# Kernel optimization log

Measured on AMD Instinct MI355X. Metric: run time of the kernel, lower is better.

## Reference

```python
import jax, jax.numpy as jnp
import numpy as np
from jax import lax

BN_EPS = 1e-5
DELTA_FRAC = 0.7


def ternarize(t):
    """Per-row (dim 0) ternarization: delta = 0.7*mean|t_i|, alpha = mean of |t_i| above delta."""
    B = t.shape[0]
    flat = t.reshape(B, -1)                       # [B, n]
    absf = jnp.abs(flat)
    n = flat.shape[1]
    d = DELTA_FRAC * absf.sum(axis=1) / n         # [B]
    mask = absf > d[:, None]                      # strict >, matching torch code
    count = mask.sum(axis=1).astype(flat.dtype)
    alpha = (absf * mask).sum(axis=1) / count     # [B]
    tern = jnp.where(flat > d[:, None], 1.0, 0.0) + jnp.where(flat < -d[:, None], -1.0, 0.0)
    return (tern * alpha[:, None]).reshape(t.shape)


def conv2d(x, w, b):
    out = lax.conv_general_dilated(x, w, window_strides=(1, 1), padding='VALID',
                                   dimension_numbers=('NCHW', 'OIHW', 'NCHW'))
    return out + b[None, :, None, None]


def maxpool2(x):
    return lax.reduce_window(x, -jnp.inf, lax.max, (1, 1, 2, 2), (1, 1, 2, 2), 'VALID')


def batchnorm_eval(x, gamma, beta):
    # eval-mode BN with running_mean=0, running_var=1
    inv = 1.0 / np.sqrt(1.0 + BN_EPS)
    return x * (gamma[None, :, None, None] * inv) + beta[None, :, None, None]


def setup_inputs() -> dict:
    key = jax.random.key(0)
    ks = jax.random.split(key, 12)
    B = 2048
    inp = {
        'x': jax.random.normal(ks[0], (B, 1, 28, 28), dtype=jnp.float32),
        'conv1_w': jax.random.normal(ks[1], (32, 1, 5, 5), dtype=jnp.float32) * 0.1,
        'conv1_b': jax.random.normal(ks[2], (32,), dtype=jnp.float32) * 0.1,
        'bn1_g': jax.random.normal(ks[3], (32,), dtype=jnp.float32) * 0.1 + 1.0,
        'bn1_b': jax.random.normal(ks[4], (32,), dtype=jnp.float32) * 0.1,
        'conv2_w': jax.random.normal(ks[5], (64, 32, 5, 5), dtype=jnp.float32) * 0.05,
        'conv2_b': jax.random.normal(ks[6], (64,), dtype=jnp.float32) * 0.1,
        'bn2_g': jax.random.normal(ks[7], (64,), dtype=jnp.float32) * 0.1 + 1.0,
        'bn2_b': jax.random.normal(ks[8], (64,), dtype=jnp.float32) * 0.1,
        'fc1_w': jax.random.normal(ks[9], (512, 1024), dtype=jnp.float32) * 0.03,
        'fc1_b': jax.random.normal(ks[10], (512,), dtype=jnp.float32) * 0.1,
        'fc2_w': jax.random.normal(ks[11], (10, 512), dtype=jnp.float32) * 0.05,
        'fc2_b': jnp.zeros((10,), dtype=jnp.float32),
    }
    return inp


def reference(x, conv1_w, conv1_b, bn1_g, bn1_b, conv2_w, conv2_b, bn2_g, bn2_b,
              fc1_w, fc1_b, fc2_w, fc2_b):
    h = ternarize(conv2d(x, conv1_w, conv1_b))            # [B,32,24,24]
    h = jax.nn.relu(maxpool2(batchnorm_eval(h, bn1_g, bn1_b)))  # [B,32,12,12]
    h = ternarize(conv2d(h, conv2_w, conv2_b))            # [B,64,8,8]
    h = jax.nn.relu(maxpool2(batchnorm_eval(h, bn2_g, bn2_b)))  # [B,64,4,4]
    h = h.reshape(-1, 1024)
    h = jax.nn.relu(ternarize(h @ fc1_w.T + fc1_b))       # [B,512]
    out = ternarize(h @ fc2_w.T + fc2_b)                  # [B,10]
    return out
```

## Files before the change

kernel.cpp:

```cpp
#include <hip/hip_runtime.h>

#define BATCH 2048

__device__ __forceinline__ float blockReduceSumF(float v, float* red, int tid, int nwaves) {
  #pragma unroll
  for (int off = 32; off > 0; off >>= 1) v += __shfl_xor(v, off);
  __syncthreads();
  if ((tid & 63) == 0) red[tid >> 6] = v;
  __syncthreads();
  if (tid == 0) {
    float s = red[0];
    for (int i = 1; i < nwaves; i++) s += red[i];
    red[31] = s;
  }
  __syncthreads();
  return red[31];
}

__device__ __forceinline__ float2 blockReduceSum2F(float a, float b, float* red, int tid, int nwaves) {
  #pragma unroll
  for (int off = 32; off > 0; off >>= 1) { a += __shfl_xor(a, off); b += __shfl_xor(b, off); }
  __syncthreads();
  if ((tid & 63) == 0) { red[tid >> 6] = a; red[(tid >> 6) + 16] = b; }
  __syncthreads();
  if (tid == 0) {
    float sa = red[0], sb = red[16];
    for (int i = 1; i < nwaves; i++) { sa += red[i]; sb += red[16 + i]; }
    red[30] = sa; red[31] = sb;
  }
  __syncthreads();
  return make_float2(red[30], red[31]);
}

__device__ __forceinline__ float groupReduce4w(float v, float* seg, int tj) {
  #pragma unroll
  for (int off = 32; off > 0; off >>= 1) v += __shfl_xor(v, off);
  __syncthreads();
  if ((tj & 63) == 0) seg[tj >> 6] = v;
  __syncthreads();
  return (seg[0] + seg[1]) + (seg[2] + seg[3]);
}

__global__ void k0_w2t(const float* __restrict__ w2, float* __restrict__ w2t) {
  int i = blockIdx.x * 256 + threadIdx.x;
  if (i >= 51200) return;
  int c2 = i / 800;
  int r = i - c2 * 800;
  w2t[r * 64 + c2] = w2[i];
}

__global__ __launch_bounds__(512, 6) void k1_conv1(
    const float* __restrict__ x, const float* __restrict__ w1, const float* __restrict__ b1,
    signed char* __restrict__ s1full, float* __restrict__ alpha1) {
  __shared__ float xs[784];
  __shared__ float wsm[800];
  __shared__ float red[32];

  const int tid = threadIdx.x;
  const int smp = blockIdx.x;

  for (int j = tid; j < 784; j += 512) xs[j] = x[smp * 784 + j];
  for (int j = tid; j < 800; j += 512) wsm[j] = w1[j];
  __syncthreads();

  const int c = tid >> 4;
  const int g = tid & 15;
  const float bias = b1[c];
  const float* wc = &wsm[c * 25];

  float a[36];
  float asum = 0.0f;
  #pragma unroll
  for (int tt = 0; tt < 3; tt++) {
    const int t = g + (tt << 4);
    const int r = t >> 1;
    const int hx = (t & 1) * 12;
    float acc[12];
    #pragma unroll
    for (int i = 0; i < 12; i++) acc[i] = bias;
    #pragma unroll
    for (int ky = 0; ky < 5; ky++) {
      const float* xp = &xs[(r + ky) * 28 + hx];
      float xrow[16];
      *(float4*)&xrow[0]  = *(const float4*)&xp[0];
      *(float4*)&xrow[4]  = *(const float4*)&xp[4];
      *(float4*)&xrow[8]  = *(const float4*)&xp[8];
      *(float4*)&xrow[12] = *(const float4*)&xp[12];
      #pragma unroll
      for (int kx = 0; kx < 5; kx++) {
        const float w = wc[ky * 5 + kx];
        #pragma unroll
        for (int i = 0; i < 12; i++) acc[i] = fmaf(xrow[i + kx], w, acc[i]);
      }
    }
    #pragma unroll
    for (int i = 0; i < 12; i++) { a[tt * 12 + i] = acc[i]; asum += fabsf(acc[i]); }
  }

  float tot = blockReduceSumF(asum, red, tid, 8);
  float delta = (0.7f * tot) / 18432.0f;

  float msum = 0.0f, mcnt = 0.0f;
  #pragma unroll
  for (int i = 0; i < 36; i++) {
    float fa = fabsf(a[i]);
    if (fa > delta) { msum += fa; mcnt += 1.0f; }
  }
  float2 mm = blockReduceSum2F(msum, mcnt, red, tid, 8);
  if (tid == 0) alpha1[smp] = (mm.y > 0.0f) ? (mm.x / mm.y) : 0.0f;

  signed char* sp = s1full + (size_t)smp * 18432 + c * 576 + g * 12;
  #pragma unroll
  for (int tt = 0; tt < 3; tt++) {
    #pragma unroll
    for (int i = 0; i < 12; i++) {
      float v = a[tt * 12 + i];
      int sv = (v > delta) ? 1 : ((v < -delta) ? -1 : 0);
      sp[tt * 192 + i] = (signed char)sv;
    }
  }
}

__global__ __launch_bounds__(256, 6) void k2_conv2(
    const signed char* __restrict__ s1full, const float* __restrict__ alpha1,
    const float* __restrict__ w2t, const float* __restrict__ b2,
    const float* __restrict__ g1, const float* __restrict__ bt1,
    signed char* __restrict__ s2full, float* __restrict__ alpha2) {
  __shared__ float pooled[4608];
  __shared__ float g1l[32], bt1l[32];
  __shared__ float red[32];

  const int tid = threadIdx.x;
  const int smp = blockIdx.x;
  const float BNINV = (float)(1.0 / sqrt(1.0 + 1e-5));

  if (tid < 32) { g1l[tid] = g1[tid] * BNINV; bt1l[tid] = bt1[tid]; }
  __syncthreads();

  const float a1 = alpha1[smp];
  for (int j = tid; j < 4608; j += 256) {
    int cc = j / 144;
    int r = j - cc * 144;
    int py = r / 12;
    int px = r - py * 12;
    const signed char* sp = s1full + (size_t)smp * 18432 + cc * 576 + (py * 2) * 24 + px * 2;
    float m = -1e30f;
    #pragma unroll
    for (int dy = 0; dy < 2; dy++)
      #pragma unroll
      for (int dx = 0; dx < 2; dx++) {
        float v = ((float)sp[dy * 24 + dx] * a1) * g1l[cc] + bt1l[cc];
        m = (v > m) ? v : m;
      }
    pooled[j] = (m > 0.0f) ? m : 0.0f;
  }
  __syncthreads();

  const int c2 = tid >> 2;
  const int q = tid & 3;
  const int r0 = q << 1;
  const float bias = b2[c2];
  float acc0[8], acc1[8];
  #pragma unroll
  for (int i = 0; i < 8; i++) { acc0[i] = bias; acc1[i] = bias; }

  for (int cc = 0; cc < 32; cc++) {
    const float* wt = w2t + cc * 1600 + c2;
    const float* pb = &pooled[cc * 144];
    float rows[2][12];
    *(float4*)&rows[0][0] = *(const float4*)&pb[r0 * 12];
    *(float4*)&rows[0][4] = *(const float4*)&pb[r0 * 12 + 4];
    *(float4*)&rows[0][8] = *(const float4*)&pb[r0 * 12 + 8];
    #pragma unroll
    for (int ky = 0; ky < 5; ky++) {
      float* B = rows[(ky + 1) & 1];
      const float* bp = &pb[(r0 + ky + 1) * 12];
      *(float4*)&B[0] = *(const float4*)&bp[0];
      *(float4*)&B[4] = *(const float4*)&bp[4];
      *(float4*)&B[8] = *(const float4*)&bp[8];
      const float* A = rows[ky & 1];
      #pragma unroll
      for (int kx = 0; kx < 5; kx++) {
        const float w = wt[(ky * 5 + kx) << 6];
        #pragma unroll
        for (int ox = 0; ox < 8; ox++) acc0[ox] = fmaf(A[ox + kx], w, acc0[ox]);
        #pragma unroll
        for (int ox = 0; ox < 8; ox++) acc1[ox] = fmaf(B[ox + kx], w, acc1[ox]);
      }
    }
  }

  float asum = 0.0f;
  #pragma unroll
  for (int i = 0; i < 8; i++) asum += fabsf(acc0[i]) + fabsf(acc1[i]);
  float tot = blockReduceSumF(asum, red, tid, 4);
  float delta = (0.7f * tot) / 4096.0f;

  float msum = 0.0f, mcnt = 0.0f;
  #pragma unroll
  for (int i = 0; i < 8; i++) {
    float f0 = fabsf(acc0[i]);
    if (f0 > delta) { msum += f0; mcnt += 1.0f; }
    float f1 = fabsf(acc1[i]);
    if (f1 > delta) { msum += f1; mcnt += 1.0f; }
  }
  float2 mm = blockReduceSum2F(msum, mcnt, red, tid, 4);
  if (tid == 0) alpha2[smp] = (mm.y > 0.0f) ? (mm.x / mm.y) : 0.0f;

  signed char* so = s2full + (size_t)smp * 4096 + c2 * 64 + r0 * 8;
  #pragma unroll
  for (int ox = 0; ox < 8; ox++) {
    float v = acc0[ox];
    so[ox] = (signed char)((v > delta) ? 1 : ((v < -delta) ? -1 : 0));
  }
  #pragma unroll
  for (int ox = 0; ox < 8; ox++) {
    float v = acc1[ox];
    so[8 + ox] = (signed char)((v > delta) ? 1 : ((v < -delta) ? -1 : 0));
  }
}

__global__ void k0_transpose(const float* __restrict__ w1f, float* __restrict__ w1t) {
  int i = blockIdx.x * 256 + threadIdx.x;
  int k = i >> 9;
  int o = i & 511;
  w1t[i] = w1f[o * 1024 + k];
}

__global__ __launch_bounds__(1024, 4) void k3_fc(
    const signed char* __restrict__ s2full, const float* __restrict__ alpha2,
    const float* __restrict__ w1t, const float* __restrict__ f1b,
    const float* __restrict__ w2f, const float* __restrict__ f2b,
    const float* __restrict__ g2, const float* __restrict__ bt2,
    float* __restrict__ out) {
  __shared__ float S[16384];
  __shared__ float fco[4][512];
  __shared__ float g2l[64], bt2l[64];
  __shared__ float redm[4][4];
  __shared__ float out2[4][10];

  const int tid = threadIdx.x;
  const int blk = blockIdx.x;
  const float BNINV = (float)(1.0 / sqrt(1.0 + 1e-5));

  if (tid < 64) { g2l[tid] = g2[tid] * BNINV; bt2l[tid] = bt2[tid]; }
  __syncthreads();

  float* h4 = S;
  for (int e = tid; e < 4096; e += 1024) {
    int j = e >> 2;
    int s = e & 3;
    int cc = j >> 4;
    int r = j & 15;
    int py = r >> 2;
    int px = r & 3;
    const signed char* sp = s2full + (size_t)(blk * 4 + s) * 4096 + cc * 64 + (py * 2) * 8 + px * 2;
    float a2 = alpha2[blk * 4 + s];
    float m = -1e30f;
    #pragma unroll
    for (int dy = 0; dy < 2; dy++)
      #pragma unroll
      for (int dx = 0; dx < 2; dx++) {
        float v = ((float)sp[dy * 8 + dx] * a2) * g2l[cc] + bt2l[cc];
        m = (v > m) ? v : m;
      }
    h4[j * 4 + s] = (m > 0.0f) ? m : 0.0f;
  }
  __syncthreads();

  const int kp = tid >> 7;
  const int og = tid & 127;
  float a00=0,a01=0,a02=0,a03=0, a10=0,a11=0,a12=0,a13=0;
  float a20=0,a21=0,a22=0,a23=0, a30=0,a31=0,a32=0,a33=0;
  const float4* w4 = (const float4*)w1t;
  const float4* h44 = (const float4*)h4;
  const int kbase = kp << 7;
  for (int kk = 0; kk < 128; kk++) {
    const int k = kbase + kk;
    const float4 wv = w4[(k << 7) + og];
    const float4 hv = h44[k];
    a00 = fmaf(hv.x, wv.x, a00); a01 = fmaf(hv.y, wv.x, a01);
    a02 = fmaf(hv.z, wv.x, a02); a03 = fmaf(hv.w, wv.x, a03);
    a10 = fmaf(hv.x, wv.y, a10); a11 = fmaf(hv.y, wv.y, a11);
    a12 = fmaf(hv.z, wv.y, a12); a13 = fmaf(hv.w, wv.y, a13);
    a20 = fmaf(hv.x, wv.z, a20); a21 = fmaf(hv.y, wv.z, a21);
    a22 = fmaf(hv.z, wv.z, a22); a23 = fmaf(hv.w, wv.z, a23);
    a30 = fmaf(hv.x, wv.w, a30); a31 = fmaf(hv.y, wv.w, a31);
    a32 = fmaf(hv.z, wv.w, a32); a33 = fmaf(hv.w, wv.w, a33);
  }
  __syncthreads();
  {
    float4* p4 = (float4*)S;
    const int base = (kp << 9) + (og << 2);
    p4[base + 0] = make_float4(a00, a01, a02, a03);
    p4[base + 1] = make_float4(a10, a11, a12, a13);
    p4[base + 2] = make_float4(a20, a21, a22, a23);
    p4[base + 3] = make_float4(a30, a31, a32, a33);
  }
  __syncthreads();

  for (int p = tid; p < 2048; p += 1024) {
    int o = p >> 2;
    int s = p & 3;
    float v = S[p];
    #pragma unroll
    for (int kp2 = 1; kp2 < 8; kp2++) v += S[kp2 * 2048 + p];
    fco[s][o] = v + f1b[o];
  }
  __syncthreads();

  float (*h3)[512] = (float(*)[512])S;
  const int sg = tid >> 8;
  const int tj = tid & 255;
  float v0 = fco[sg][tj];
  float v1 = fco[sg][tj + 256];
  float av0 = fabsf(v0), av1 = fabsf(v1);
  float tot = groupReduce4w(av0 + av1, redm[sg], tj);
  float delta = (0.7f * tot) / 512.0f;
  float m0 = (av0 > delta) ? av0 : 0.0f;
  float m1 = (av1 > delta) ? av1 : 0.0f;
  float msum = groupReduce4w(m0 + m1, redm[sg], tj);
  float mcnt = groupReduce4w(((av0 > delta) ? 1.0f : 0.0f) + ((av1 > delta) ? 1.0f : 0.0f),
                             redm[sg], tj);
  float alpha3 = (mcnt > 0.0f) ? (msum / mcnt) : 0.0f;
  {
    float t0 = (v0 > delta) ? 1.0f : ((v0 < -delta) ? -1.0f : 0.0f);
    float hv0 = t0 * alpha3;
    h3[sg][tj] = (hv0 > 0.0f) ? hv0 : 0.0f;
    float t1 = (v1 > delta) ? 1.0f : ((v1 < -delta) ? -1.0f : 0.0f);
    float hv1 = t1 * alpha3;
    h3[sg][tj + 256] = (hv1 > 0.0f) ? hv1 : 0.0f;
  }
  __syncthreads();

  const int lane = tid & 63;
  const int wid = tid >> 6;
  for (int t = wid; t < 40; t += 16) {
    int s = t / 10;
    int o = t - s * 10;
    float acc = 0.0f;
    #pragma unroll
    for (int m = 0; m < 8; m++) {
      int j = lane + (m << 6);
      acc = fmaf(h3[s][j], w2f[o * 512 + j], acc);
    }
    #pragma unroll
    for (int off = 32; off > 0; off >>= 1) acc += __shfl_xor(acc, off);
    if (lane == 0) out2[s][o] = acc + f2b[o];
  }
  __syncthreads();

  if (tid < 4) {
    int s = tid;
    float t2 = 0.0f;
    for (int i = 0; i < 10; i++) t2 += fabsf(out2[s][i]);
    float d = (0.7f * t2) / 10.0f;
    float ms = 0.0f, mc = 0.0f;
    for (int i = 0; i < 10; i++) {
      float a = fabsf(out2[s][i]);
      if (a > d) { ms += a; mc += 1.0f; }
    }
    float al = (mc > 0.0f) ? (ms / mc) : 0.0f;
    for (int i = 0; i < 10; i++) {
      float vv = out2[s][i];
      float sv = (vv > d) ? 1.0f : ((vv < -d) ? -1.0f : 0.0f);
      out[(size_t)(blk * 4 + s) * 10 + i] = sv * al;
    }
  }
}

__global__ void k_marker(float* __restrict__ out, int n, float val) {
  int i = blockIdx.x * 256 + threadIdx.x;
  if (i < n) out[i] = val;
}

extern "C" void kernel_launch(void* const* d_in, const int* in_sizes, int n_in,
                              void* d_out, int out_size, void* d_ws, size_t ws_size,
                              hipStream_t stream) {
  float* out = (float*)d_out;

  static const int expect[13] = {1605632, 800, 32, 32, 32, 51200, 64, 64, 64,
                                 524288, 512, 5120, 10};
  float marker = 0.0f;
  if (n_in != 13) marker = 304.0f;
  else {
    for (int i = 0; i < 13; i++)
      if (in_sizes[i] != expect[i]) { marker = 320.0f + 16.0f * i; break; }
  }
  if (marker == 0.0f && out_size != 20480) marker = 560.0f;

  float* alpha1 = (float*)d_ws;
  float* alpha2 = alpha1 + BATCH;
  float* w2t    = alpha2 + BATCH;
  signed char* s1full = (signed char*)(w2t + 51200);
  signed char* s2full = s1full + (size_t)BATCH * 18432;
  size_t needed = (size_t)((s2full + (size_t)BATCH * 4096) - (signed char*)d_ws);
  if (marker == 0.0f && ws_size < needed) marker = 576.0f;

  if (marker != 0.0f) {
    k_marker<<<dim3((out_size + 255) / 256), dim3(256), 0, stream>>>(out, out_size, marker);
    return;
  }

  const float* x   = (const float*)d_in[0];
  const float* c1w = (const float*)d_in[1];
  const float* c1b = (const float*)d_in[2];
  const float* g1  = (const float*)d_in[3];
  const float* bt1 = (const float*)d_in[4];
  const float* c2w = (const float*)d_in[5];
  const float* c2b = (const float*)d_in[6];
  const float* g2  = (const float*)d_in[7];
  const float* bt2 = (const float*)d_in[8];
  const float* f1w = (const float*)d_in[9];
  const float* f1b = (const float*)d_in[10];
  const float* f2w = (const float*)d_in[11];
  const float* f2b = (const float*)d_in[12];

  float* w1t = (float*)s1full;

  k0_w2t<<<dim3(200), dim3(256), 0, stream>>>(c2w, w2t);
  k1_conv1<<<dim3(BATCH), dim3(512), 0, stream>>>(x, c1w, c1b, s1full, alpha1);
  k2_conv2<<<dim3(BATCH), dim3(256), 0, stream>>>(s1full, alpha1, w2t, c2b, g1, bt1, s2full, alpha2);
  k0_transpose<<<dim3(2048), dim3(256), 0, stream>>>(f1w, w1t);
  k3_fc<<<dim3(BATCH / 4), dim3(1024), 0, stream>>>(s2full, alpha2, w1t, f1b, f2w, f2b, g2, bt2, out);
}
```

Measured before the change: 381.6 us.

## Repack conv2 weights for float4 register prefetch and pack ternary stores

Conv2 weights are relaid out per input channel and output channel, padded to 28 floats, so each thread loads its 25 taps as seven float4s into registers. The next channel's weights are prefetched (double-buffered) while the current channel computes. This replaces the 25 scalar global loads per channel issued in the inner loop. Conv1 and conv2 ternary outputs are packed into 32-bit and 128-bit stores, and the pooling loads use char2 reads. Occupancy hint drops from 6 to 4 blocks, and the prefetch uses extra registers.

```diff
diff --git a/kernel.cpp b/kernel.cpp
--- a/kernel.cpp
+++ b/kernel.cpp
@@ -41,12 +41,14 @@
   return (seg[0] + seg[1]) + (seg[2] + seg[3]);
 }
 
-__global__ void k0_w2t(const float* __restrict__ w2, float* __restrict__ w2t) {
+__global__ void k0_w2t(const float* __restrict__ w2, float* __restrict__ w2t2) {
   int i = blockIdx.x * 256 + threadIdx.x;
-  if (i >= 51200) return;
-  int c2 = i / 800;
-  int r = i - c2 * 800;
-  w2t[r * 64 + c2] = w2[i];
+  if (i >= 57344) return;
+  int cc = i / 1792;
+  int r = i - cc * 1792;
+  int c2 = r / 28;
+  int k = r - c2 * 28;
+  w2t2[i] = (k < 25) ? w2[c2 * 800 + cc * 25 + k] : 0.0f;
 }
 
 __global__ __launch_bounds__(512, 6) void k1_conv1(
@@ -112,18 +114,55 @@
   signed char* sp = s1full + (size_t)smp * 18432 + c * 576 + g * 12;
   #pragma unroll
   for (int tt = 0; tt < 3; tt++) {
+    int s_[12];
     #pragma unroll
     for (int i = 0; i < 12; i++) {
       float v = a[tt * 12 + i];
-      int sv = (v > delta) ? 1 : ((v < -delta) ? -1 : 0);
-      sp[tt * 192 + i] = (signed char)sv;
-    }
-  }
-}
-
-__global__ __launch_bounds__(256, 6) void k2_conv2(
+      s_[i] = (v > delta) ? 1 : ((v < -delta) ? -1 : 0);
+    }
+    unsigned u0 = (s_[0] & 0xFF) | ((s_[1] & 0xFF) << 8) | ((s_[2] & 0xFF) << 16) |
+                  (((unsigned)(s_[3] & 0xFF)) << 24);
+    unsigned u1 = (s_[4] & 0xFF) | ((s_[5] & 0xFF) << 8) | ((s_[6] & 0xFF) << 16) |
+                  (((unsigned)(s_[7] & 0xFF)) << 24);
+    unsigned u2 = (s_[8] & 0xFF) | ((s_[9] & 0xFF) << 8) | ((s_[10] & 0xFF) << 16) |
+                  (((unsigned)(s_[11] & 0xFF)) << 24);
+    unsigned* wq = (unsigned*)(sp + tt * 192);
+    wq[0] = u0; wq[1] = u1; wq[2] = u2;
+  }
+}
+
+__device__ __forceinline__ void conv_body(const float* __restrict__ pb, int r0,
+    float4 W0, float4 W1, float4 W2, float4 W3, float4 W4, float4 W5, float4 W6,
+    float* __restrict__ acc0, float* __restrict__ acc1) {
+  const float wk[25] = {W0.x, W0.y, W0.z, W0.w, W1.x, W1.y, W1.z, W1.w,
+                        W2.x, W2.y, W2.z, W2.w, W3.x, W3.y, W3.z, W3.w,
+                        W4.x, W4.y, W4.z, W4.w, W5.x, W5.y, W5.z, W5.w, W6.x};
+  float rows[2][12];
+  *(float4*)&rows[0][0] = *(const float4*)&pb[r0 * 12];
+  *(float4*)&rows[0][4] = *(const float4*)&pb[r0 * 12 + 4];
+  *(float4*)&rows[0][8] = *(const float4*)&pb[r0 * 12 + 8];
+  #pragma unroll
+  for (int ky = 0; ky < 5; ky++) {
+    float* B = rows[(ky + 1) & 1];
+    const float* bp = &pb[(r0 + ky + 1) * 12];
+    *(float4*)&B[0] = *(const float4*)&bp[0];
+    *(float4*)&B[4] = *(const float4*)&bp[4];
+    *(float4*)&B[8] = *(const float4*)&bp[8];
+    const float* A = rows[ky & 1];
+    #pragma unroll
+    for (int kx = 0; kx < 5; kx++) {
+      const float w = wk[ky * 5 + kx];
+      #pragma unroll
+      for (int ox = 0; ox < 8; ox++) acc0[ox] = fmaf(A[ox + kx], w, acc0[ox]);
+      #pragma unroll
+      for (int ox = 0; ox < 8; ox++) acc1[ox] = fmaf(B[ox + kx], w, acc1[ox]);
+    }
+  }
+}
+
+__global__ __launch_bounds__(256, 4) void k2_conv2(
     const signed char* __restrict__ s1full, const float* __restrict__ alpha1,
-    const float* __restrict__ w2t, const float* __restrict__ b2,
+    const float* __restrict__ w2t2, const float* __restrict__ b2,
     const float* __restrict__ g1, const float* __restrict__ bt1,
     signed char* __restrict__ s2full, float* __restrict__ alpha2) {
   __shared__ float pooled[4608];
@@ -139,19 +178,18 @@
 
   const float a1 = alpha1[smp];
   for (int j = tid; j < 4608; j += 256) {
-    int cc = j / 144;
-    int r = j - cc * 144;
+    int ci = j / 144;
+    int r = j - ci * 144;
     int py = r / 12;
     int px = r - py * 12;
-    const signed char* sp = s1full + (size_t)smp * 18432 + cc * 576 + (py * 2) * 24 + px * 2;
+    const signed char* sp = s1full + (size_t)smp * 18432 + ci * 576 + (py * 2) * 24 + px * 2;
+    char2 t0 = *(const char2*)sp;
+    char2 t1 = *(const char2*)(sp + 24);
     float m = -1e30f;
-    #pragma unroll
-    for (int dy = 0; dy < 2; dy++)
-      #pragma unroll
-      for (int dx = 0; dx < 2; dx++) {
-        float v = ((float)sp[dy * 24 + dx] * a1) * g1l[cc] + bt1l[cc];
-        m = (v > m) ? v : m;
-      }
+    { float v = ((float)t0.x * a1) * g1l[ci] + bt1l[ci]; m = (v > m) ? v : m; }
+    { float v = ((float)t0.y * a1) * g1l[ci] + bt1l[ci]; m = (v > m) ? v : m; }
+    { float v = ((float)t1.x * a1) * g1l[ci] + bt1l[ci]; m = (v > m) ? v : m; }
+    { float v = ((float)t1.y * a1) * g1l[ci] + bt1l[ci]; m = (v > m) ? v : m; }
     pooled[j] = (m > 0.0f) ? m : 0.0f;
   }
   __syncthreads();
@@ -164,30 +202,18 @@
   #pragma unroll
   for (int i = 0; i < 8; i++) { acc0[i] = bias; acc1[i] = bias; }
 
-  for (int cc = 0; cc < 32; cc++) {
-    const float* wt = w2t + cc * 1600 + c2;
-    const float* pb = &pooled[cc * 144];
-    float rows[2][12];
-    *(float4*)&rows[0][0] = *(const float4*)&pb[r0 * 12];
-    *(float4*)&rows[0][4] = *(const float4*)&pb[r0 * 12 + 4];
-    *(float4*)&rows[0][8] = *(const float4*)&pb[r0 * 12 + 8];
-    #pragma unroll
-    for (int ky = 0; ky < 5; ky++) {
-      float* B = rows[(ky + 1) & 1];
-      const float* bp = &pb[(r0 + ky + 1) * 12];
-      *(float4*)&B[0] = *(const float4*)&bp[0];
-      *(float4*)&B[4] = *(const float4*)&bp[4];
-      *(float4*)&B[8] = *(const float4*)&bp[8];
-      const float* A = rows[ky & 1];
-      #pragma unroll
-      for (int kx = 0; kx < 5; kx++) {
-        const float w = wt[(ky * 5 + kx) << 6];
-        #pragma unroll
-        for (int ox = 0; ox < 8; ox++) acc0[ox] = fmaf(A[ox + kx], w, acc0[ox]);
-        #pragma unroll
-        for (int ox = 0; ox < 8; ox++) acc1[ox] = fmaf(B[ox + kx], w, acc1[ox]);
-      }
-    }
+  const float4* wbase = ((const float4*)w2t2) + c2 * 7;
+  const float4* wp = wbase;
+  float4 A0 = wp[0], A1 = wp[1], A2 = wp[2], A3 = wp[3], A4 = wp[4], A5 = wp[5], A6 = wp[6];
+  #pragma unroll 1
+  for (int cc = 0; cc < 32; cc += 2) {
+    const float4* wn = wp + 448;
+    float4 B0 = wn[0], B1 = wn[1], B2 = wn[2], B3 = wn[3], B4 = wn[4], B5 = wn[5], B6 = wn[6];
+    conv_body(&pooled[cc * 144], r0, A0, A1, A2, A3, A4, A5, A6, acc0, acc1);
+    const float4* wn2 = (cc < 30) ? (wp + 896) : wbase;
+    A0 = wn2[0]; A1 = wn2[1]; A2 = wn2[2]; A3 = wn2[3]; A4 = wn2[4]; A5 = wn2[5]; A6 = wn2[6];
+    conv_body(&pooled[(cc + 1) * 144], r0, B0, B1, B2, B3, B4, B5, B6, acc0, acc1);
+    wp += 896;
   }
 
   float asum = 0.0f;
@@ -207,17 +233,26 @@
   float2 mm = blockReduceSum2F(msum, mcnt, red, tid, 4);
   if (tid == 0) alpha2[smp] = (mm.y > 0.0f) ? (mm.x / mm.y) : 0.0f;
 
-  signed char* so = s2full + (size_t)smp * 4096 + c2 * 64 + r0 * 8;
+  int t_[16];
   #pragma unroll
   for (int ox = 0; ox < 8; ox++) {
     float v = acc0[ox];
-    so[ox] = (signed char)((v > delta) ? 1 : ((v < -delta) ? -1 : 0));
+    t_[ox] = (v > delta) ? 1 : ((v < -delta) ? -1 : 0);
   }
   #pragma unroll
   for (int ox = 0; ox < 8; ox++) {
     float v = acc1[ox];
-    so[8 + ox] = (signed char)((v > delta) ? 1 : ((v < -delta) ? -1 : 0));
-  }
+    t_[8 + ox] = (v > delta) ? 1 : ((v < -delta) ? -1 : 0);
+  }
+  unsigned u0 = (t_[0] & 0xFF) | ((t_[1] & 0xFF) << 8) | ((t_[2] & 0xFF) << 16) |
+                (((unsigned)(t_[3] & 0xFF)) << 24);
+  unsigned u1 = (t_[4] & 0xFF) | ((t_[5] & 0xFF) << 8) | ((t_[6] & 0xFF) << 16) |
+                (((unsigned)(t_[7] & 0xFF)) << 24);
+  unsigned u2 = (t_[8] & 0xFF) | ((t_[9] & 0xFF) << 8) | ((t_[10] & 0xFF) << 16) |
+                (((unsigned)(t_[11] & 0xFF)) << 24);
+  unsigned u3 = (t_[12] & 0xFF) | ((t_[13] & 0xFF) << 8) | ((t_[14] & 0xFF) << 16) |
+                (((unsigned)(t_[15] & 0xFF)) << 24);
+  *(uint4*)(s2full + (size_t)smp * 4096 + c2 * 64 + r0 * 8) = make_uint4(u0, u1, u2, u3);
 }
 
 __global__ void k0_transpose(const float* __restrict__ w1f, float* __restrict__ w1t) {
@@ -391,8 +426,8 @@
 
   float* alpha1 = (float*)d_ws;
   float* alpha2 = alpha1 + BATCH;
-  float* w2t    = alpha2 + BATCH;
-  signed char* s1full = (signed char*)(w2t + 51200);
+  float* w2t2   = alpha2 + BATCH;
+  signed char* s1full = (signed char*)(w2t2 + 57344);
   signed char* s2full = s1full + (size_t)BATCH * 18432;
   size_t needed = (size_t)((s2full + (size_t)BATCH * 4096) - (signed char*)d_ws);
   if (marker == 0.0f && ws_size < needed) marker = 576.0f;
@@ -418,9 +453,9 @@
 
   float* w1t = (float*)s1full;
 
-  k0_w2t<<<dim3(200), dim3(256), 0, stream>>>(c2w, w2t);
+  k0_w2t<<<dim3(224), dim3(256), 0, stream>>>(c2w, w2t2);
   k1_conv1<<<dim3(BATCH), dim3(512), 0, stream>>>(x, c1w, c1b, s1full, alpha1);
-  k2_conv2<<<dim3(BATCH), dim3(256), 0, stream>>>(s1full, alpha1, w2t, c2b, g1, bt1, s2full, alpha2);
+  k2_conv2<<<dim3(BATCH), dim3(256), 0, stream>>>(s1full, alpha1, w2t2, c2b, g1, bt1, s2full, alpha2);
   k0_transpose<<<dim3(2048), dim3(256), 0, stream>>>(f1w, w1t);
   k3_fc<<<dim3(BATCH / 4), dim3(1024), 0, stream>>>(s2full, alpha2, w1t, f1b, f2w, f2b, g2, bt2, out);
 }
```

Result: slower. 459.2 us (+20.4%).
